# Performance work log

Measured on AMD Instinct MI355X. Metric: run time of the kernel, lower is better.

Reference implementation:

```python
import jax, jax.numpy as jnp
import numpy as np

L, D, H, DFF, P, B = 10, 512, 8, 1536, 16, 1024
DK = D // H
SQRT_DK = float(np.sqrt(DK))

# board geometry constants (square index -> rank/file/diag)
_pos = np.arange(64)
FILES = _pos % 8
RANKS = _pos // 8
DIAGS = RANKS + FILES
ADIAGS = RANKS - FILES + 7
RIDX = np.clip(RANKS[:, None] - RANKS[None, :], -7, 7) + 7  # [64,64]
FIDX = np.clip(FILES[:, None] - FILES[None, :], -7, 7) + 7  # [64,64]


def setup_inputs() -> dict:
    key = jax.random.key(0)
    ks = iter(jax.random.split(key, 40))
    n = lambda shape, s=0.02: (jax.random.normal(next(ks), shape, jnp.float32) * s)
    inp = {
        'x': jax.random.normal(next(ks), (B, 64, P), jnp.float32),
        'emb_W': n((P, D)), 'emb_b': jnp.zeros((D,), jnp.float32),
        'cls': n((1, 1, D)), 'abs_pos': n((1, 64, D)),
        'file_tab': n((8, D)), 'rank_tab': n((8, D)),
        'diag_tab': n((15, D)), 'anti_tab': n((15, D)),
        'rel_bias': n((L, 15, 15, H)),
        'Wq': n((L, D, D)), 'bq': jnp.zeros((L, D)),
        'Wk': n((L, D, D)), 'bk': jnp.zeros((L, D)),
        'Wv': n((L, D, D)), 'bv': jnp.zeros((L, D)),
        'Wo': n((L, D, D)), 'bo': jnp.zeros((L, D)),
        'ln1_g': jnp.ones((L, D)), 'ln1_b': jnp.zeros((L, D)),
        'ln2_g': jnp.ones((L, D)), 'ln2_b': jnp.zeros((L, D)),
        'W1': n((L, D, 2 * DFF)), 'b1': jnp.zeros((L, 2 * DFF)),
        'W2': n((L, DFF, D)), 'b2': jnp.zeros((L, D)),
        'fln_g': jnp.ones((D,)), 'fln_b': jnp.zeros((D,)),
        'pol_W': n((D, 72)), 'pol_b': jnp.zeros((72,)),
        'v1_W': n((D, D // 2)), 'v1_b': jnp.zeros((D // 2,)),
        'v2_W': n((D // 2, 128)), 'v2_b': jnp.zeros((128,)),
        'v3_W': n((128, 1)), 'v3_b': jnp.zeros((1,)),
    }
    return inp


def _ln(x, g, b):
    m = x.mean(-1, keepdims=True)
    v = ((x - m) ** 2).mean(-1, keepdims=True)
    return (x - m) * jax.lax.rsqrt(v + 1e-5) * g + b


def _gelu(x):
    return jax.nn.gelu(x, approximate=False)  # torch F.gelu default (erf)


def reference(x, emb_W, emb_b, cls, abs_pos, file_tab, rank_tab, diag_tab, anti_tab,
              rel_bias, Wq, bq, Wk, bk, Wv, bv, Wo, bo, ln1_g, ln1_b, ln2_g, ln2_b,
              W1, b1, W2, b2, fln_g, fln_b, pol_W, pol_b,
              v1_W, v1_b, v2_W, v2_b, v3_W, v3_b):
    Bn = x.shape[0]
    # per-square embedding + chess positional encoding
    emb = x @ emb_W + emb_b                                   # [B,64,D]
    pe = abs_pos + file_tab[FILES] + rank_tab[RANKS] + diag_tab[DIAGS] + anti_tab[ADIAGS]
    t = emb + pe
    t = jnp.concatenate([jnp.broadcast_to(cls, (Bn, 1, D)), t], axis=1)  # [B,65,D]
    for i in range(L):
        h = _ln(t, ln1_g[i], ln1_b[i])
        q = (h @ Wq[i] + bq[i]).reshape(Bn, 65, H, DK).transpose(0, 2, 1, 3)
        k = (h @ Wk[i] + bk[i]).reshape(Bn, 65, H, DK).transpose(0, 2, 1, 3)
        v = (h @ Wv[i] + bv[i]).reshape(Bn, 65, H, DK).transpose(0, 2, 1, 3)
        scores = jnp.einsum('bhqd,bhkd->bhqk', q, k) / SQRT_DK
        bias = rel_bias[i][RIDX, FIDX]                        # [64,64,H]
        bias = jnp.pad(bias.transpose(2, 0, 1), ((0, 0), (1, 0), (1, 0)))  # zero bias for CLS
        scores = scores + bias[None]
        a = jax.nn.softmax(scores, axis=-1)
        ctx = jnp.einsum('bhqk,bhkd->bhqd', a, v).transpose(0, 2, 1, 3).reshape(Bn, 65, D)
        t = t + (ctx @ Wo[i] + bo[i])
        h = _ln(t, ln2_g[i], ln2_b[i])
        p = h @ W1[i] + b1[i]
        x1, x2 = jnp.split(p, 2, axis=-1)
        t = t + (_gelu(x1) * x2) @ W2[i] + b2[i]
    t = _ln(t, fln_g, fln_b)
    policy = (t[:, 1:] @ pol_W + pol_b).reshape(Bn, -1)       # [B,4608]
    vh = t[:, 0]                                              # CLS token
    value = jnp.tanh(_gelu(_gelu(vh @ v1_W + v1_b) @ v2_W + v2_b) @ v3_W + v3_b)  # [B,1]
    return policy, value
```

## Files before the change

### kernel.cpp

```cpp
#include <hip/hip_runtime.h>
#include <hip/hip_bf16.h>
#include <math.h>


typedef short short8 __attribute__((ext_vector_type(8)));
typedef float f32x4 __attribute__((ext_vector_type(4)));

#define NLAYER 10
#define DMODEL 512
#define NHEAD 8
#define BATCH 1024
#define SEQ 65

#define WT_QKV   0L
#define WT_WO    7864320L
#define WT_W1    10485760L
#define WT_W2    26214400L
#define WT_BQKV  34078720L
#define WT_BO    34094080L
#define WT_B1    34099200L
#define WT_B2    34129920L
#define WT_TOTAL 34135040L

__device__ __forceinline__ float bf2f(ushort u){ return __uint_as_float(((unsigned)u)<<16); }
__device__ __forceinline__ ushort f2bf(float f){
  unsigned u = __float_as_uint(f);
  unsigned r = (u + 0x7fffu + ((u>>16)&1u)) >> 16;
  return (ushort)r;
}
__device__ __forceinline__ float gelu_exact(float x){
  return 0.5f*x*(1.0f+erff(x*0.70710678118654752440f));
}
__device__ __forceinline__ void gl16(ushort* lds, const ushort* g){
  __builtin_amdgcn_global_load_lds(
      (const unsigned int __attribute__((address_space(1)))*)g,
      (unsigned int __attribute__((address_space(3)))*)lds,
      16, 0, 0);
}

__global__ void prep_qkv(const float* __restrict__ Wq, const float* __restrict__ Wk,
                         const float* __restrict__ Wv, ushort* __restrict__ wT)
{
  long idx = (long)blockIdx.x*256 + threadIdx.x;
  if(idx >= 7864320L) return;
  int l = (int)(idx/786432L);
  long r = idx - (long)l*786432L;
  int n = (int)(r>>9), k = (int)(r&511);
  float v;
  if(n<512)       v = Wq[(long)l*262144 + (long)k*512 + n];
  else if(n<1024) v = Wk[(long)l*262144 + (long)k*512 + (n-512)];
  else            v = Wv[(long)l*262144 + (long)k*512 + (n-1024)];
  wT[WT_QKV + idx] = f2bf(v);
}
__global__ void prep_wo(const float* __restrict__ Wo, ushort* __restrict__ wT)
{
  long idx = (long)blockIdx.x*256 + threadIdx.x;
  if(idx >= 2621440L) return;
  int l = (int)(idx/262144L);
  long r = idx - (long)l*262144L;
  int n = (int)(r>>9), k = (int)(r&511);
  wT[WT_WO + idx] = f2bf(Wo[(long)l*262144 + (long)k*512 + n]);
}
__global__ void prep_w1(const float* __restrict__ W1, ushort* __restrict__ wT)
{
  long idx = (long)blockIdx.x*256 + threadIdx.x;
  if(idx >= 15728640L) return;
  int l = (int)(idx/1572864L);
  long r = idx - (long)l*1572864L;
  int n = (int)(r>>9), k = (int)(r&511);
  int j = n>>1;
  int src = (n&1) ? 1536+j : j;
  wT[WT_W1 + idx] = f2bf(W1[(long)l*1572864 + (long)k*3072 + src]);
}
__global__ void prep_w2(const float* __restrict__ W2, ushort* __restrict__ wT)
{
  long idx = (long)blockIdx.x*256 + threadIdx.x;
  if(idx >= 7864320L) return;
  int l = (int)(idx/786432L);
  long r = idx - (long)l*786432L;
  int n = (int)(r/1536), k = (int)(r - (long)n*1536);
  wT[WT_W2 + idx] = f2bf(W2[(long)l*786432 + (long)k*512 + n]);
}
__global__ void prep_bias(const float* __restrict__ bq, const float* __restrict__ bk,
                          const float* __restrict__ bv, const float* __restrict__ bo,
                          const float* __restrict__ b1, const float* __restrict__ b2,
                          ushort* __restrict__ wT)
{
  int idx = blockIdx.x*256 + threadIdx.x;
  if(idx >= 56320) return;
  long o = WT_BQKV + idx;
  float v;
  if(o < WT_BO){
    int i = idx;
    int l = i/1536, n = i - l*1536;
    if(n<512) v=bq[l*512+n]; else if(n<1024) v=bk[l*512+n-512]; else v=bv[l*512+n-1024];
  } else if(o < WT_B1){
    int i = (int)(o - WT_BO);
    v = bo[i];
  } else if(o < WT_B2){
    int i = (int)(o - WT_B1);
    int l = i/3072, n = i - l*3072;
    int j=n>>1; int src=(n&1)?1536+j:j;
    v = b1[l*3072+src];
  } else {
    int i = (int)(o - WT_B2);
    v = b2[i];
  }
  wT[o] = f2bf(v);
}

__global__ __launch_bounds__(64) void embed_kernel(
    const float* __restrict__ x, const float* __restrict__ emb_W,
    const float* __restrict__ emb_b, const float* __restrict__ cls,
    const float* __restrict__ abs_pos, const float* __restrict__ file_tab,
    const float* __restrict__ rank_tab, const float* __restrict__ diag_tab,
    const float* __restrict__ anti_tab, float* __restrict__ t, long xoff)
{
  long tok = blockIdx.x;
  int lane = threadIdx.x;
  long b = tok/SEQ;
  int s = (int)(tok - b*SEQ);
  float* out = t + tok*DMODEL;
  if(s==0){
    #pragma unroll
    for(int j=0;j<8;j++){ int d=lane*8+j; out[d]=cls[d]; }
    return;
  }
  int p = s-1;
  int f = p&7, r = p>>3;
  int dg = r+f, ad = r-f+7;
  float xv[16];
  #pragma unroll
  for(int k=0;k<16;k++) xv[k]=x[xoff + (b*64+p)*16+k];
  #pragma unroll
  for(int j=0;j<8;j++){
    int d = lane*8+j;
    float acc = emb_b[d] + abs_pos[p*512+d] + file_tab[f*512+d]
              + rank_tab[r*512+d] + diag_tab[dg*512+d] + anti_tab[ad*512+d];
    #pragma unroll
    for(int k=0;k<16;k++) acc += xv[k]*emb_W[k*512+d];
    out[d]=acc;
  }
}

__global__ __launch_bounds__(64) void ln_kernel(const float* __restrict__ t, ushort* __restrict__ h,
                                                const float* __restrict__ g, const float* __restrict__ b,
                                                long goff)
{
  long tok = blockIdx.x;
  int lane = threadIdx.x;
  const float* row = t + tok*DMODEL;
  float4 v0 = *reinterpret_cast<const float4*>(row + lane*8);
  float4 v1 = *reinterpret_cast<const float4*>(row + lane*8 + 4);
  float x[8] = {v0.x,v0.y,v0.z,v0.w,v1.x,v1.y,v1.z,v1.w};
  float s=0.f, ss=0.f;
  #pragma unroll
  for(int j=0;j<8;j++){ s+=x[j]; ss+=x[j]*x[j]; }
  #pragma unroll
  for(int off=32;off>=1;off>>=1){ s+=__shfl_down(s,off); ss+=__shfl_down(ss,off); }
  s=__shfl(s,0); ss=__shfl(ss,0);
  float mean = s*(1.0f/512.0f);
  float var  = ss*(1.0f/512.0f) - mean*mean;
  float rs = rsqrtf(fmaxf(var,0.0f) + 1e-5f);
  #pragma unroll
  for(int j=0;j<8;j++){
    int d=lane*8+j;
    h[tok*DMODEL+d] = f2bf((x[j]-mean)*rs*g[goff+d] + b[goff+d]);
  }
}

template<int EPI>
__global__ __launch_bounds__(256,2) void gemm_bt(
    const ushort* __restrict__ A, long lda,
    const ushort* __restrict__ BT,
    const ushort* __restrict__ bias,
    ushort* __restrict__ Cb, float* __restrict__ Cf,
    long ldc, int K)
{
  __shared__ __align__(16) ushort As[128*32];
  __shared__ __align__(16) ushort Bs[128*32];
  const int tid = threadIdx.x;
  const int w = tid>>6, lane = tid&63, q = lane>>4, lr = lane&15;
  const int wm = (w>>1)*64, wn = (w&1)*64;
  const long mBase = (long)blockIdx.y*128, nBase = (long)blockIdx.x*128;

  f32x4 acc[4][4];
  #pragma unroll
  for(int i=0;i<4;i++)
    #pragma unroll
    for(int j=0;j<4;j++) acc[i][j]=(f32x4)(0.0f);

  const int idx0=tid, idx1=tid+256;
  const int ar0=idx0>>2, ac0=(idx0&3)*8;
  const int ar1=idx1>>2, ac1=(idx1&3)*8;

  const ushort* gA0 = A  + (mBase+ar0)*lda     + ac0;
  const ushort* gA1 = A  + (mBase+ar1)*lda     + ac1;
  const ushort* gB0 = BT + (nBase+ar0)*(long)K + ac0;
  const ushort* gB1 = BT + (nBase+ar1)*(long)K + ac1;
  ushort* lA0 = As + idx0*8;
  ushort* lA1 = As + idx1*8;
  ushort* lB0 = Bs + idx0*8;
  ushort* lB1 = Bs + idx1*8;

  for(int k0=0;k0<K;k0+=32){
    __syncthreads();
    gl16(lA0, gA0 + k0);
    gl16(lA1, gA1 + k0);
    gl16(lB0, gB0 + k0);
    gl16(lB1, gB1 + k0);
    __syncthreads();
    short8 af[4], bfr[4];
    #pragma unroll
    for(int mt=0;mt<4;mt++) af[mt]=*reinterpret_cast<const short8*>(As + (wm+mt*16+lr)*32 + q*8);
    #pragma unroll
    for(int nt=0;nt<4;nt++) bfr[nt]=*reinterpret_cast<const short8*>(Bs + (wn+nt*16+lr)*32 + q*8);
    #pragma unroll
    for(int mt=0;mt<4;mt++)
      #pragma unroll
      for(int nt=0;nt<4;nt++)
        acc[mt][nt]=__builtin_amdgcn_mfma_f32_16x16x32_bf16(af[mt],bfr[nt],acc[mt][nt],0,0,0);
  }

  #pragma unroll
  for(int nt=0;nt<4;nt++){
    long n = nBase+wn+nt*16+lr;
    float bv = bf2f(bias[n]);
    #pragma unroll
    for(int mt=0;mt<4;mt++){
      #pragma unroll
      for(int r=0;r<4;r++){
        long m = mBase+wm+mt*16+q*4+r;
        float v = acc[mt][nt][r]+bv;
        if constexpr (EPI==0){
          Cb[m*ldc+n]=f2bf(v);
        } else if constexpr (EPI==1){
          Cf[m*ldc+n]+=v;
        } else {
          float partner = __shfl_xor(v,1);
          if(!(lane&1)) Cb[m*ldc + (n>>1)] = f2bf(gelu_exact(v)*partner);
        }
      }
    }
  }
}

__global__ __launch_bounds__(256) void attn_kernel(const ushort* __restrict__ qkv,
                                                   const float* __restrict__ rel_bias,
                                                   ushort* __restrict__ ctx, int layer)
{
  int bh = blockIdx.x;
  long b = bh>>3;
  int h = bh&7;
  __shared__ __align__(16) ushort Qb[80*72];
  __shared__ __align__(16) ushort Kb[80*72];
  __shared__ __align__(16) ushort Vt[64*104];
  __shared__ __align__(16) float  S [80*81];
  __shared__ __align__(16) ushort Pb[80*104];
  __shared__ float relb[225];
  const long tokBase = b*SEQ;
  const int tid = threadIdx.x;
  const int w = tid>>6, lane = tid&63, q = lane>>4, lr = lane&15;

  for(int idx=tid; idx<SEQ*8; idx+=256){
    int s = idx>>3, c8 = (idx&7)<<3;
    long base = (tokBase+s)*1536 + h*64 + c8;
    *reinterpret_cast<short8*>(&Qb[s*72 + c8]) = *reinterpret_cast<const short8*>(&qkv[base]);
    *reinterpret_cast<short8*>(&Kb[s*72 + c8]) = *reinterpret_cast<const short8*>(&qkv[base+512]);
    short8 v = *reinterpret_cast<const short8*>(&qkv[base+1024]);
    #pragma unroll
    for(int j=0;j<8;j++) Vt[(c8+j)*104 + s] = (ushort)v[j];
  }
  for(int idx=tid; idx<64*32; idx+=256){
    int d = idx>>5, s = 65+(idx&31);
    Vt[d*104 + s] = 0;
  }
  if(tid<225) relb[tid] = rel_bias[((long)layer*225 + tid)*8 + h];
  __syncthreads();

  for(int tt=w; tt<25; tt+=4){
    int mt = tt/5, nt = tt - mt*5;
    f32x4 acc = (f32x4)(0.0f);
    #pragma unroll
    for(int ks=0;ks<2;ks++){
      short8 af = *reinterpret_cast<const short8*>(&Qb[(mt*16+lr)*72 + ks*32 + q*8]);
      short8 bf = *reinterpret_cast<const short8*>(&Kb[(nt*16+lr)*72 + ks*32 + q*8]);
      acc = __builtin_amdgcn_mfma_f32_16x16x32_bf16(af, bf, acc, 0,0,0);
    }
    int col = nt*16 + lr;
    #pragma unroll
    for(int r=0;r<4;r++)
      S[(mt*16 + q*4 + r)*81 + col] = acc[r]*0.125f;
  }
  __syncthreads();

  if(tid < SEQ){
    int qi = tid;
    float* srow = S + qi*81;
    int pq = qi-1;
    float mx = -1e30f;
    for(int k=0;k<SEQ;k++){
      float s = srow[k];
      if(qi>0 && k>0){
        int pk = k-1;
        int ridx = (pq>>3)-(pk>>3)+7, fidx = (pq&7)-(pk&7)+7;
        s += relb[ridx*15+fidx];
      }
      srow[k] = s;
      mx = fmaxf(mx, s);
    }
    float sum = 0.f;
    for(int k=0;k<SEQ;k++){ float e = __expf(srow[k]-mx); srow[k]=e; sum+=e; }
    float inv = 1.0f/sum;
    ushort* prow = Pb + qi*104;
    for(int k=0;k<SEQ;k++) prow[k] = f2bf(srow[k]*inv);
    for(int k=SEQ;k<96;k++) prow[k] = 0;
  }
  __syncthreads();

  for(int tt=w; tt<20; tt+=4){
    int mt = tt>>2, nt = tt&3;
    f32x4 acc = (f32x4)(0.0f);
    #pragma unroll
    for(int ks=0;ks<3;ks++){
      short8 af = *reinterpret_cast<const short8*>(&Pb[(mt*16+lr)*104 + ks*32 + q*8]);
      short8 bf = *reinterpret_cast<const short8*>(&Vt[(nt*16+lr)*104 + ks*32 + q*8]);
      acc = __builtin_amdgcn_mfma_f32_16x16x32_bf16(af, bf, acc, 0,0,0);
    }
    int col = nt*16 + lr;
    #pragma unroll
    for(int r=0;r<4;r++){
      int row = mt*16 + q*4 + r;
      if(row < SEQ)
        ctx[(tokBase+row)*512 + h*64 + col] = f2bf(acc[r]);
    }
  }
}

__global__ __launch_bounds__(128) void policy_kernel(const ushort* __restrict__ h,
                                                     const float* __restrict__ pol_W,
                                                     const float* __restrict__ pol_b,
                                                     float* __restrict__ out, long b0)
{
  int bp = blockIdx.x;
  long bl = bp>>6;
  int p = bp&63;
  const ushort* hrow = h + (bl*SEQ + 1 + p)*DMODEL;
  __shared__ float hl[DMODEL];
  for(int d=threadIdx.x; d<DMODEL; d+=128) hl[d]=bf2f(hrow[d]);
  __syncthreads();
  int j = threadIdx.x;
  if(j<72){
    float acc = pol_b[j];
    for(int k=0;k<DMODEL;k++) acc += hl[k]*pol_W[k*72+j];
    out[(b0+bl)*4608 + (long)p*72 + j] = acc;
  }
}

__global__ __launch_bounds__(256) void value_kernel(const ushort* __restrict__ h,
                                                    const float* __restrict__ v1_W, const float* __restrict__ v1_b,
                                                    const float* __restrict__ v2_W, const float* __restrict__ v2_b,
                                                    const float* __restrict__ v3_W, const float* __restrict__ v3_b,
                                                    float* __restrict__ out, long b0)
{
  long bl = blockIdx.x;
  int tid = threadIdx.x;
  __shared__ float vh[512], a1[256], a2[128];
  const ushort* hrow = h + bl*SEQ*DMODEL;
  for(int d=tid; d<512; d+=256) vh[d]=bf2f(hrow[d]);
  __syncthreads();
  {
    float acc = v1_b[tid];
    for(int k=0;k<512;k++) acc += vh[k]*v1_W[k*256+tid];
    a1[tid]=gelu_exact(acc);
  }
  __syncthreads();
  if(tid<128){
    float acc = v2_b[tid];
    for(int k=0;k<256;k++) acc += a1[k]*v2_W[k*128+tid];
    a2[tid]=gelu_exact(acc);
  }
  __syncthreads();
  if(tid==0){
    float acc = v3_b[0];
    for(int k=0;k<128;k++) acc += a2[k]*v3_W[k];
    out[(long)BATCH*4608 + b0 + bl] = tanhf(acc);
  }
}

extern "C" void kernel_launch(void* const* d_in, const int* in_sizes, int n_in,
                              void* d_out, int out_size, void* d_ws, size_t ws_size,
                              hipStream_t stream)
{
  const float* x        = (const float*)d_in[0];
  const float* emb_W    = (const float*)d_in[1];
  const float* emb_b    = (const float*)d_in[2];
  const float* cls      = (const float*)d_in[3];
  const float* abs_pos  = (const float*)d_in[4];
  const float* file_tab = (const float*)d_in[5];
  const float* rank_tab = (const float*)d_in[6];
  const float* diag_tab = (const float*)d_in[7];
  const float* anti_tab = (const float*)d_in[8];
  const float* rel_bias = (const float*)d_in[9];
  const float* Wq  = (const float*)d_in[10];
  const float* bq  = (const float*)d_in[11];
  const float* Wk  = (const float*)d_in[12];
  const float* bk  = (const float*)d_in[13];
  const float* Wv  = (const float*)d_in[14];
  const float* bv  = (const float*)d_in[15];
  const float* Wo  = (const float*)d_in[16];
  const float* bo  = (const float*)d_in[17];
  const float* ln1_g = (const float*)d_in[18];
  const float* ln1_b = (const float*)d_in[19];
  const float* ln2_g = (const float*)d_in[20];
  const float* ln2_b = (const float*)d_in[21];
  const float* W1  = (const float*)d_in[22];
  const float* b1  = (const float*)d_in[23];
  const float* W2  = (const float*)d_in[24];
  const float* b2  = (const float*)d_in[25];
  const float* fln_g = (const float*)d_in[26];
  const float* fln_b = (const float*)d_in[27];
  const float* pol_W = (const float*)d_in[28];
  const float* pol_b = (const float*)d_in[29];
  const float* v1_W  = (const float*)d_in[30];
  const float* v1_b  = (const float*)d_in[31];
  const float* v2_W  = (const float*)d_in[32];
  const float* v2_b  = (const float*)d_in[33];
  const float* v3_W  = (const float*)d_in[34];
  const float* v3_b  = (const float*)d_in[35];
  float* out = (float*)d_out;

  int nchunk = 4;
  if(ws_size >= (size_t)477214720) nchunk = 1;
  else if(ws_size >= (size_t)272742400) nchunk = 2;
  const int bch = BATCH / nchunk;
  const long mch = (long)bch * SEQ;

  char* ws = (char*)d_ws;
  float*  t    = (float*)ws;  ws += (size_t)mch*DMODEL*4;
  ushort* h    = (ushort*)ws; ws += (size_t)mch*DMODEL*2;
  ushort* buf1 = (ushort*)ws; ws += (size_t)mch*1536*2;
  ushort* wT   = (ushort*)ws; ws += (size_t)WT_TOTAL*2;
  (void)ws_size; (void)in_sizes; (void)n_in; (void)out_size;

  prep_qkv<<<(7864320+255)/256,256,0,stream>>>(Wq,Wk,Wv,wT);
  prep_wo <<<(2621440+255)/256,256,0,stream>>>(Wo,wT);
  prep_w1 <<<(15728640+255)/256,256,0,stream>>>(W1,wT);
  prep_w2 <<<(7864320+255)/256,256,0,stream>>>(W2,wT);
  prep_bias<<<(56320+255)/256,256,0,stream>>>(bq,bk,bv,bo,b1,b2,wT);

  const int gy = (int)(mch/128);
  for(int c=0;c<nchunk;c++){
    long b0 = (long)c*bch;
    embed_kernel<<<(int)mch,64,0,stream>>>(x, emb_W, emb_b, cls, abs_pos,
                                      file_tab, rank_tab, diag_tab, anti_tab, t, b0*64*16);
    for(int l=0;l<NLAYER;l++){
      ln_kernel<<<(int)mch,64,0,stream>>>(t, h, ln1_g, ln1_b, l*512);
      gemm_bt<0><<<dim3(12,gy),256,0,stream>>>(h, 512, wT+WT_QKV+(long)l*786432,
                                                wT+WT_BQKV+l*1536, buf1, nullptr, 1536, 512);
      attn_kernel<<<bch*NHEAD,256,0,stream>>>(buf1, rel_bias, h, l);
      gemm_bt<1><<<dim3(4,gy),256,0,stream>>>(h, 512, wT+WT_WO+(long)l*262144,
                                               wT+WT_BO+l*512, nullptr, t, 512, 512);
      ln_kernel<<<(int)mch,64,0,stream>>>(t, h, ln2_g, ln2_b, l*512);
      gemm_bt<2><<<dim3(24,gy),256,0,stream>>>(h, 512, wT+WT_W1+(long)l*1572864,
                                                wT+WT_B1+l*3072, buf1, nullptr, 1536, 512);
      gemm_bt<1><<<dim3(4,gy),256,0,stream>>>(buf1, 1536, wT+WT_W2+(long)l*786432,
                                               wT+WT_B2+l*512, nullptr, t, 512, 1536);
    }
    ln_kernel<<<(int)mch,64,0,stream>>>(t, h, fln_g, fln_b, 0);
    policy_kernel<<<bch*64,128,0,stream>>>(h, pol_W, pol_b, out, b0);
    value_kernel<<<bch,256,0,stream>>>(h, v1_W, v1_b, v2_W, v2_b, v3_W, v3_b, out, b0);
  }
}
```

Baseline: 13.15 ms.

## Use MFMA GEMM for policy head, parallelize softmax, batch LN rows per block

Replaces the scalar per-token policy kernel with the bf16 MFMA gemm_bt using a new epilogue that scatters into the policy output, padding the policy weights to 128 columns in a prep kernel. The attention softmax now spreads each row over 4 lanes with shuffle reductions, so all 256 threads work instead of 65. LayerNorm handles 4 tokens per 256-thread block, which cuts block count and launch overhead. The policy head now rounds activations and weights to bf16, a small precision change, and the workspace grows to hold the padded weights.

```diff
diff --git a/kernel.cpp b/kernel.cpp
--- a/kernel.cpp
+++ b/kernel.cpp
@@ -20,7 +20,9 @@
 #define WT_BO    34094080L
 #define WT_B1    34099200L
 #define WT_B2    34129920L
-#define WT_TOTAL 34135040L
+#define WT_POL   34135040L
+#define WT_BPOL  34200576L
+#define WT_TOTAL 34200704L
 
 __device__ __forceinline__ float bf2f(ushort u){ return __uint_as_float(((unsigned)u)<<16); }
 __device__ __forceinline__ ushort f2bf(float f){
@@ -108,6 +110,19 @@
   }
   wT[o] = f2bf(v);
 }
+__global__ void prep_pol(const float* __restrict__ pol_W, const float* __restrict__ pol_b,
+                         ushort* __restrict__ wT)
+{
+  int idx = blockIdx.x*256 + threadIdx.x;
+  if(idx >= 65536+128) return;
+  if(idx < 65536){
+    int n = idx>>9, k = idx&511;
+    wT[WT_POL + idx] = f2bf(n<72 ? pol_W[k*72+n] : 0.0f);
+  } else {
+    int n = idx - 65536;
+    wT[WT_BPOL + n] = f2bf(n<72 ? pol_b[n] : 0.0f);
+  }
+}
 
 __global__ __launch_bounds__(64) void embed_kernel(
     const float* __restrict__ x, const float* __restrict__ emb_W,
@@ -143,12 +158,12 @@
   }
 }
 
-__global__ __launch_bounds__(64) void ln_kernel(const float* __restrict__ t, ushort* __restrict__ h,
-                                                const float* __restrict__ g, const float* __restrict__ b,
-                                                long goff)
-{
-  long tok = blockIdx.x;
-  int lane = threadIdx.x;
+__global__ __launch_bounds__(256) void ln_kernel(const float* __restrict__ t, ushort* __restrict__ h,
+                                                 const float* __restrict__ g, const float* __restrict__ b,
+                                                 long goff)
+{
+  long tok = (long)blockIdx.x*4 + (threadIdx.x>>6);
+  int lane = threadIdx.x&63;
   const float* row = t + tok*DMODEL;
   float4 v0 = *reinterpret_cast<const float4*>(row + lane*8);
   float4 v1 = *reinterpret_cast<const float4*>(row + lane*8 + 4);
@@ -236,9 +251,13 @@
           Cb[m*ldc+n]=f2bf(v);
         } else if constexpr (EPI==1){
           Cf[m*ldc+n]+=v;
-        } else {
+        } else if constexpr (EPI==2){
           float partner = __shfl_xor(v,1);
           if(!(lane&1)) Cb[m*ldc + (n>>1)] = f2bf(gelu_exact(v)*partner);
+        } else {
+          long bl = m/65;
+          int p = (int)(m - bl*65) - 1;
+          if(p>=0 && n<72) Cf[bl*4608 + (long)p*72 + n] = v;
         }
       }
     }
@@ -294,27 +313,33 @@
   }
   __syncthreads();
 
-  if(tid < SEQ){
-    int qi = tid;
-    float* srow = S + qi*81;
-    int pq = qi-1;
-    float mx = -1e30f;
-    for(int k=0;k<SEQ;k++){
-      float s = srow[k];
-      if(qi>0 && k>0){
-        int pk = k-1;
-        int ridx = (pq>>3)-(pk>>3)+7, fidx = (pq&7)-(pk&7)+7;
-        s += relb[ridx*15+fidx];
+  {
+    int grp = tid>>2, sub = tid&3;
+    for(int qi=grp; qi<SEQ; qi+=64){
+      float* srow = S + qi*81;
+      int pq = qi-1;
+      float mx = -1e30f;
+      for(int k=sub;k<SEQ;k+=4){
+        float s = srow[k];
+        if(qi>0 && k>0){
+          int pk = k-1;
+          int ridx = (pq>>3)-(pk>>3)+7, fidx = (pq&7)-(pk&7)+7;
+          s += relb[ridx*15+fidx];
+        }
+        srow[k] = s;
+        mx = fmaxf(mx, s);
       }
-      srow[k] = s;
-      mx = fmaxf(mx, s);
-    }
-    float sum = 0.f;
-    for(int k=0;k<SEQ;k++){ float e = __expf(srow[k]-mx); srow[k]=e; sum+=e; }
-    float inv = 1.0f/sum;
-    ushort* prow = Pb + qi*104;
-    for(int k=0;k<SEQ;k++) prow[k] = f2bf(srow[k]*inv);
-    for(int k=SEQ;k<96;k++) prow[k] = 0;
+      mx = fmaxf(mx, __shfl_xor(mx,1));
+      mx = fmaxf(mx, __shfl_xor(mx,2));
+      float sum = 0.f;
+      for(int k=sub;k<SEQ;k+=4){ float e = __expf(srow[k]-mx); srow[k]=e; sum+=e; }
+      sum += __shfl_xor(sum,1);
+      sum += __shfl_xor(sum,2);
+      float inv = 1.0f/sum;
+      ushort* prow = Pb + qi*104;
+      for(int k=sub;k<SEQ;k+=4) prow[k] = f2bf(srow[k]*inv);
+      for(int k=SEQ+sub;k<96;k+=4) prow[k] = 0;
+    }
   }
   __syncthreads();
 
@@ -334,26 +359,6 @@
       if(row < SEQ)
         ctx[(tokBase+row)*512 + h*64 + col] = f2bf(acc[r]);
     }
-  }
-}
-
-__global__ __launch_bounds__(128) void policy_kernel(const ushort* __restrict__ h,
-                                                     const float* __restrict__ pol_W,
-                                                     const float* __restrict__ pol_b,
-                                                     float* __restrict__ out, long b0)
-{
-  int bp = blockIdx.x;
-  long bl = bp>>6;
-  int p = bp&63;
-  const ushort* hrow = h + (bl*SEQ + 1 + p)*DMODEL;
-  __shared__ float hl[DMODEL];
-  for(int d=threadIdx.x; d<DMODEL; d+=128) hl[d]=bf2f(hrow[d]);
-  __syncthreads();
-  int j = threadIdx.x;
-  if(j<72){
-    float acc = pol_b[j];
-    for(int k=0;k<DMODEL;k++) acc += hl[k]*pol_W[k*72+j];
-    out[(b0+bl)*4608 + (long)p*72 + j] = acc;
   }
 }
 
@@ -431,8 +436,8 @@
   float* out = (float*)d_out;
 
   int nchunk = 4;
-  if(ws_size >= (size_t)477214720) nchunk = 1;
-  else if(ws_size >= (size_t)272742400) nchunk = 2;
+  if(ws_size >= (size_t)477345792) nchunk = 1;
+  else if(ws_size >= (size_t)272873472) nchunk = 2;
   const int bch = BATCH / nchunk;
   const long mch = (long)bch * SEQ;
 
@@ -448,27 +453,30 @@
   prep_w1 <<<(15728640+255)/256,256,0,stream>>>(W1,wT);
   prep_w2 <<<(7864320+255)/256,256,0,stream>>>(W2,wT);
   prep_bias<<<(56320+255)/256,256,0,stream>>>(bq,bk,bv,bo,b1,b2,wT);
+  prep_pol <<<(65664+255)/256,256,0,stream>>>(pol_W,pol_b,wT);
 
   const int gy = (int)(mch/128);
+  const int lng = (int)(mch/4);
   for(int c=0;c<nchunk;c++){
     long b0 = (long)c*bch;
     embed_kernel<<<(int)mch,64,0,stream>>>(x, emb_W, emb_b, cls, abs_pos,
                                       file_tab, rank_tab, diag_tab, anti_tab, t, b0*64*16);
     for(int l=0;l<NLAYER;l++){
-      ln_kernel<<<(int)mch,64,0,stream>>>(t, h, ln1_g, ln1_b, l*512);
+      ln_kernel<<<lng,256,0,stream>>>(t, h, ln1_g, ln1_b, l*512);
       gemm_bt<0><<<dim3(12,gy),256,0,stream>>>(h, 512, wT+WT_QKV+(long)l*786432,
                                                 wT+WT_BQKV+l*1536, buf1, nullptr, 1536, 512);
       attn_kernel<<<bch*NHEAD,256,0,stream>>>(buf1, rel_bias, h, l);
       gemm_bt<1><<<dim3(4,gy),256,0,stream>>>(h, 512, wT+WT_WO+(long)l*262144,
                                                wT+WT_BO+l*512, nullptr, t, 512, 512);
-      ln_kernel<<<(int)mch,64,0,stream>>>(t, h, ln2_g, ln2_b, l*512);
+      ln_kernel<<<lng,256,0,stream>>>(t, h, ln2_g, ln2_b, l*512);
       gemm_bt<2><<<dim3(24,gy),256,0,stream>>>(h, 512, wT+WT_W1+(long)l*1572864,
                                                 wT+WT_B1+l*3072, buf1, nullptr, 1536, 512);
       gemm_bt<1><<<dim3(4,gy),256,0,stream>>>(buf1, 1536, wT+WT_W2+(long)l*786432,
                                                wT+WT_B2+l*512, nullptr, t, 512, 1536);
     }
-    ln_kernel<<<(int)mch,64,0,stream>>>(t, h, fln_g, fln_b, 0);
-    policy_kernel<<<bch*64,128,0,stream>>>(h, pol_W, pol_b, out, b0);
+    ln_kernel<<<lng,256,0,stream>>>(t, h, fln_g, fln_b, 0);
+    gemm_bt<3><<<dim3(1,gy),256,0,stream>>>(h, 512, wT+WT_POL,
+                                            wT+WT_BPOL, nullptr, out + b0*4608, 0, 512);
     value_kernel<<<bch,256,0,stream>>>(h, v1_W, v1_b, v2_W, v2_b, v3_W, v3_b, out, b0);
   }
 }
```

Measured after the change: 12.39 ms. 5.8% less time.
